# Optimization experiments

Measured on AMD Instinct MI355X. Metric: run time of the kernel, lower is better.

Reference implementation:

```python
import jax, jax.numpy as jnp
import numpy as np

DIM = 128
NUM_HEADS = 8
HEAD_DIM = DIM // NUM_HEADS
SCALE = HEAD_DIM ** -0.5


def setup_inputs() -> dict:
    key = jax.random.key(0)
    k0, k1, k2, k3 = jax.random.split(key, 4)
    B, N, C, H, W = 4, 8, DIM, 96, 96
    features = jax.random.normal(k0, (B, N, C, H, W), dtype=jnp.float32)
    w_qkv = jax.random.normal(k1, (C, 3 * C), dtype=jnp.float32) * (C ** -0.5)
    w_proj = jax.random.normal(k2, (C, C), dtype=jnp.float32) * (C ** -0.5)
    b_proj = jax.random.normal(k3, (C,), dtype=jnp.float32) * 0.02
    gamma = jnp.ones((C,), dtype=jnp.float32)
    beta = jnp.zeros((C,), dtype=jnp.float32)
    return {"features": features, "w_qkv": w_qkv, "w_proj": w_proj,
            "b_proj": b_proj, "gamma": gamma, "beta": beta}


def _layernorm(x, gamma, beta, eps=1e-5):
    mu = jnp.mean(x, axis=-1, keepdims=True)
    var = jnp.mean(jnp.square(x - mu), axis=-1, keepdims=True)
    return (x - mu) * jax.lax.rsqrt(var + eps) * gamma + beta


def reference(features, w_qkv, w_proj, b_proj, gamma, beta):
    B, N, C, H, W = features.shape
    residual = features
    # (B,N,C,H,W) -> (B*H*W, N, C)
    x = jnp.transpose(features, (0, 3, 4, 1, 2)).reshape(B * H * W, N, C)
    x = _layernorm(x, gamma, beta)
    qkv = (x @ w_qkv).reshape(B * H * W, N, 3, NUM_HEADS, HEAD_DIM)
    qkv = jnp.transpose(qkv, (2, 0, 3, 1, 4))  # (3, P, h, N, d)
    q, k, v = qkv[0], qkv[1], qkv[2]
    attn = jnp.einsum('phnd,phmd->phnm', q, k) * SCALE
    attn = jax.nn.softmax(attn, axis=-1)
    out = jnp.einsum('phnm,phmd->phnd', attn, v)  # (P, h, N, d)
    out = jnp.transpose(out, (0, 2, 1, 3)).reshape(B * H * W, N, C)
    out = out @ w_proj + b_proj
    out = out.reshape(B, H, W, N, C).transpose(0, 3, 4, 1, 2)
    return residual + out
```

## Files before the change

### kernel.cpp

```cpp
#include <hip/hip_runtime.h>

#define NFR 8
#define CDIM 128
#define HH 96
#define WW 96
#define NB 4
#define HWSZ 9216
#define NBLK 2304
#define NXCD 8
#define CPX (NBLK / NXCD)

typedef __attribute__((ext_vector_type(8))) short bf16x8;
typedef __attribute__((ext_vector_type(4))) float f32x4;
typedef __attribute__((ext_vector_type(2))) float f32x2;
typedef __attribute__((ext_vector_type(2))) __bf16 bf16x2;

union FragU { uint4 u; bf16x8 v; };

__device__ inline float bf2f(unsigned short h) {
    unsigned int x = ((unsigned int)h) << 16;
    float f; __builtin_memcpy(&f, &x, 4); return f;
}
__device__ inline unsigned short f2bf(float f) {
    unsigned int x; __builtin_memcpy(&x, &f, 4);
    return (unsigned short)((x + 0x7FFFu + ((x >> 16) & 1u)) >> 16);
}
__device__ inline unsigned int packbf(float a, float b) {
    return (unsigned int)f2bf(a) | ((unsigned int)f2bf(b) << 16);
}
__device__ inline unsigned int cvt2(float a, float b) {
    f32x2 f = {a, b};
    bf16x2 h = __builtin_convertvector(f, bf16x2);
    unsigned int u; __builtin_memcpy(&u, &h, 4); return u;
}
__device__ inline unsigned short cvt1(float a) {
    __bf16 h = (__bf16)a;
    unsigned short s; __builtin_memcpy(&s, &h, 2); return s;
}
__device__ inline int posmap(int c5) {
    return (c5 < 16) ? (((c5 >> 2) << 3) + (c5 & 3))
                     : ((((c5 & 15) >> 2) << 3) + 4 + (c5 & 3));
}

__global__ __launch_bounds__(256)
void repack_k(const float* __restrict__ wqkv, const float* __restrict__ wproj,
              const float* __restrict__ gamma, const float* __restrict__ beta,
              unsigned short* __restrict__ ws)
{
    int gid = blockIdx.x * 256 + threadIdx.x;
    uint4* wsq = (uint4*)ws;
    int l = gid & 63, lr = l & 15, lg = (l >> 4) & 3;
    if (gid < 8192) {
        int unit = gid >> 6;
        int col, ks, stride;
        float scale = 1.0f;
        const float* src;
        if (unit < 64) {
            int t = unit >> 2; ks = unit & 3;
            int hd = t >> 1, three = t & 1;
            col = three * 128 + hd * 16 + lr;
            src = wqkv; stride = 384;
            if (three == 0) scale = 0.25f;
        } else if (unit < 96) {
            int u2 = unit - 64; int hd = u2 >> 2; ks = u2 & 3;
            col = 256 + hd * 16 + lr;
            src = wqkv; stride = 384;
        } else {
            int u3 = unit - 96; int nt = u3 >> 2; ks = u3 & 3;
            col = nt * 16 + lr;
            src = wproj; stride = 128;
        }
        unsigned int dw[4];
        #pragma unroll
        for (int i = 0; i < 4; ++i) {
            int e0 = 2 * i, e1 = 2 * i + 1;
            int c0 = ks * 32 + lg * 4 + (e0 & 3) + ((e0 >> 2) << 4);
            int c1 = ks * 32 + lg * 4 + (e1 & 3) + ((e1 >> 2) << 4);
            dw[i] = packbf(src[c0 * stride + col] * scale, src[c1 * stride + col] * scale);
        }
        uint4 o; o.x = dw[0]; o.y = dw[1]; o.z = dw[2]; o.w = dw[3];
        wsq[gid] = o;
    } else if (gid < 8192 + 256) {
        int p = gid - 8192;
        int pp = p & 127;
        int ks = pp >> 5, pos = pp & 31;
        int c = ks * 32 + ((pos >> 3) << 2) + (pos & 3) + (((pos >> 2) & 1) << 4);
        ((float*)ws)[32768 + p] = (p < 128) ? gamma[c] : beta[c];
    }
}

__device__ inline f32x4 attn_ov(f32x4 q, f32x4 k, f32x4 v, bool valid) {
    FragU qb, kb, vb;
    qb.u.x = cvt2(q.x, q.y); qb.u.y = cvt2(q.z, q.w); qb.u.z = 0; qb.u.w = 0;
    kb.u.x = cvt2(k.x, k.y); kb.u.y = cvt2(k.z, k.w); kb.u.z = 0; kb.u.w = 0;
    vb.u.x = cvt2(v.x, v.y); vb.u.y = cvt2(v.z, v.w); vb.u.z = 0; vb.u.w = 0;
    f32x4 zz = {0,0,0,0};
    f32x4 st = __builtin_amdgcn_mfma_f32_16x16x32_bf16(kb.v, qb.v, zz, 0, 0, 0);
    float sc0 = st.x, sc1 = st.y, sc2 = st.z, sc3 = st.w;
    float m = valid ? fmaxf(fmaxf(sc0, sc1), fmaxf(sc2, sc3)) : -3.0e38f;
    m = fmaxf(m, __shfl_xor(m, 16));
    float e0 = valid ? __expf(sc0 - m) : 0.f, e1 = valid ? __expf(sc1 - m) : 0.f;
    float e2 = valid ? __expf(sc2 - m) : 0.f, e3 = valid ? __expf(sc3 - m) : 0.f;
    float sm = e0 + e1 + e2 + e3; sm += __shfl_xor(sm, 16);
    float inv = 1.f / sm;
    FragU pb;
    pb.u.x = cvt2(valid ? e0 * inv : 0.f, valid ? e1 * inv : 0.f);
    pb.u.y = cvt2(valid ? e2 * inv : 0.f, valid ? e3 * inv : 0.f);
    pb.u.z = 0; pb.u.w = 0;
    return __builtin_amdgcn_mfma_f32_16x16x32_bf16(vb.v, pb.v, zz, 0, 0, 0);
}

__global__ __launch_bounds__(256, 3)
void cfa_main(const float* __restrict__ feat, const float* __restrict__ bproj,
              const unsigned short* __restrict__ ws, float* __restrict__ outp)
{
    __shared__ uint4 xlnU4[2048];
    unsigned short* xln16 = (unsigned short*)xlnU4;
    unsigned int*   xln32 = (unsigned int*)xlnU4;

    const int tid = threadIdx.x;
    const int blk = (int)(blockIdx.x % NXCD) * CPX + (int)blockIdx.x / NXCD;
    const int wt = blk % 6, h = (blk / 6) % 96, b = blk / (6 * 96);
    const int base = ((b * NFR) * CDIM) * HWSZ + h * WW + wt * 16;

    #pragma unroll
    for (int it = 0; it < 8; ++it) {
        int t = it * 256 + tid;
        int pq = t & 3;
        int pr = t >> 2;
        int n = pr >> 6;
        int c = (pr & 63) * 2;
        const float* src = feat + base + (n * CDIM + c) * HWSZ + pq * 4;
        float4 f0 = *(const float4*)src;
        float4 f1 = *(const float4*)(src + HWSZ);
        int ks = c >> 5;
        int pos = posmap(c & 31);
        const float* a0 = (const float*)&f0;
        const float* a1 = (const float*)&f1;
        #pragma unroll
        for (int j = 0; j < 4; ++j) {
            int p = pq * 4 + j;
            int g = p >> 3, pin = p & 7;
            xln32[(g * 8192 + ks * 2048 + (pin * 8 + n) * 32 + pos) >> 1] =
                cvt2(a0[j], a1[j]);
        }
    }
    __syncthreads();

    const int wv = tid >> 6, l = tid & 63, lr = l & 15, lg = l >> 4;
    const uint4* wsq = (const uint4*)ws;

    uint4 Ac[4], Bc[4], Vc[4];
    #pragma unroll
    for (int ks = 0; ks < 4; ++ks) {
        Ac[ks] = wsq[(0 * 8 + ks) * 64 + l];
        Bc[ks] = wsq[(0 * 8 + 4 + ks) * 64 + l];
        Vc[ks] = wsq[4096 + ks * 64 + l];
    }

    {
        const float* gP = (const float*)ws + 32768;
        const float* bP = gP + 128;
        int rr = tid >> 2, ks = tid & 3;
        #pragma unroll
        for (int g = 0; g < 2; ++g) {
            int baseq = g * 1024 + ks * 256 + rr * 4;
            uint4 ch[4];
            #pragma unroll
            for (int j = 0; j < 4; ++j) ch[j] = xlnU4[baseq + ((j + rr + ks) & 3)];
            float s = 0.f, ss = 0.f;
            #pragma unroll
            for (int j = 0; j < 4; ++j) {
                const unsigned short* e = (const unsigned short*)&ch[j];
                #pragma unroll
                for (int b8 = 0; b8 < 8; ++b8) { float x = bf2f(e[b8]); s += x; ss += x * x; }
            }
            s += __shfl_xor(s, 1); ss += __shfl_xor(ss, 1);
            s += __shfl_xor(s, 2); ss += __shfl_xor(ss, 2);
            float mu = s * (1.f / 128.f);
            float var = ss * (1.f / 128.f) - mu * mu;
            float rstd = rsqrtf(var + 1e-5f);
            #pragma unroll
            for (int j = 0; j < 4; ++j) {
                int cj = (j + rr + ks) & 3;
                const unsigned short* e = (const unsigned short*)&ch[j];
                unsigned int dw[4];
                #pragma unroll
                for (int i = 0; i < 4; ++i) {
                    int p0 = cj * 8 + 2 * i, p1 = p0 + 1;
                    float x0 = (bf2f(e[2 * i])     - mu) * rstd * gP[ks * 32 + p0] + bP[ks * 32 + p0];
                    float x1 = (bf2f(e[2 * i + 1]) - mu) * rstd * gP[ks * 32 + p1] + bP[ks * 32 + p1];
                    dw[i] = cvt2(x0, x1);
                }
                uint4 o; o.x = dw[0]; o.y = dw[1]; o.z = dw[2]; o.w = dw[3];
                xlnU4[baseq + cj] = o;
            }
        }
    }

    FragU xf0[4], xf1[4];
    #pragma unroll
    for (int ks = 0; ks < 4; ++ks) {
        xf0[ks].u = xlnU4[ks * 256 + (wv * 16 + lr) * 4 + lg];
        xf1[ks].u = xlnU4[1024 + ks * 256 + (wv * 16 + lr) * 4 + lg];
    }
    __syncthreads();

    const bool valid = ((lg >> 1) == (lr >> 3));
    FragU pa0[4], pa1[4];
    #pragma unroll
    for (int ks = 0; ks < 4; ++ks) {
        pa0[ks].u.x = 0; pa0[ks].u.y = 0; pa0[ks].u.z = 0; pa0[ks].u.w = 0;
        pa1[ks].u.x = 0; pa1[ks].u.y = 0; pa1[ks].u.z = 0; pa1[ks].u.w = 0;
    }

    uint4 PBc[4];
    float biasc;
    #pragma unroll
    for (int hd = 0; hd < 8; ++hd) {
        uint4 An[4], Bn[4], Vn[4];
        if (hd < 7) {
            #pragma unroll
            for (int ks = 0; ks < 4; ++ks) {
                An[ks] = wsq[((hd + 1) * 8 + ks) * 64 + l];
                Bn[ks] = wsq[((hd + 1) * 8 + 4 + ks) * 64 + l];
                Vn[ks] = wsq[4096 + ((hd + 1) * 4 + ks) * 64 + l];
            }
        } else {
            #pragma unroll
            for (int ks = 0; ks < 4; ++ks) PBc[ks] = wsq[6144 + ks * 64 + l];
            biasc = bproj[lr];
        }
        f32x4 q0 = {0,0,0,0}, k0 = {0,0,0,0}, v0 = {0,0,0,0};
        f32x4 q1 = {0,0,0,0}, k1 = {0,0,0,0}, v1 = {0,0,0,0};
        #pragma unroll
        for (int ks = 0; ks < 4; ++ks) {
            FragU A, B, V2; A.u = Ac[ks]; B.u = Bc[ks]; V2.u = Vc[ks];
            q0 = __builtin_amdgcn_mfma_f32_16x16x32_bf16(A.v,  xf0[ks].v, q0, 0, 0, 0);
            k0 = __builtin_amdgcn_mfma_f32_16x16x32_bf16(B.v,  xf0[ks].v, k0, 0, 0, 0);
            q1 = __builtin_amdgcn_mfma_f32_16x16x32_bf16(A.v,  xf1[ks].v, q1, 0, 0, 0);
            k1 = __builtin_amdgcn_mfma_f32_16x16x32_bf16(B.v,  xf1[ks].v, k1, 0, 0, 0);
            v0 = __builtin_amdgcn_mfma_f32_16x16x32_bf16(xf0[ks].v, V2.v, v0, 0, 0, 0);
            v1 = __builtin_amdgcn_mfma_f32_16x16x32_bf16(xf1[ks].v, V2.v, v1, 0, 0, 0);
        }
        f32x4 o0 = attn_ov(q0, k0, v0, valid);
        f32x4 o1 = attn_ov(q1, k1, v1, valid);
        if ((hd & 1) == 0) {
            pa0[hd >> 1].u.x = cvt2(o0.x, o0.y); pa0[hd >> 1].u.y = cvt2(o0.z, o0.w);
            pa1[hd >> 1].u.x = cvt2(o1.x, o1.y); pa1[hd >> 1].u.y = cvt2(o1.z, o1.w);
        } else {
            pa0[hd >> 1].u.z = cvt2(o0.x, o0.y); pa0[hd >> 1].u.w = cvt2(o0.z, o0.w);
            pa1[hd >> 1].u.z = cvt2(o1.x, o1.y); pa1[hd >> 1].u.w = cvt2(o1.z, o1.w);
        }
        if (hd < 7) {
            #pragma unroll
            for (int ks = 0; ks < 4; ++ks) { Ac[ks] = An[ks]; Bc[ks] = Bn[ks]; Vc[ks] = Vn[ks]; }
        }
    }

    unsigned short* out_t = xln16;
    #pragma unroll
    for (int nt = 0; nt < 8; ++nt) {
        uint4 PBn[4]; float biasn;
        if (nt < 7) {
            #pragma unroll
            for (int ks = 0; ks < 4; ++ks) PBn[ks] = wsq[6144 + ((nt + 1) * 4 + ks) * 64 + l];
            biasn = bproj[(nt + 1) * 16 + lr];
        }
        f32x4 a0 = {0,0,0,0}, a1 = {0,0,0,0};
        #pragma unroll
        for (int ks = 0; ks < 4; ++ks) {
            FragU B; B.u = PBc[ks];
            a0 = __builtin_amdgcn_mfma_f32_16x16x32_bf16(pa0[ks].v, B.v, a0, 0, 0, 0);
            a1 = __builtin_amdgcn_mfma_f32_16x16x32_bf16(pa1[ks].v, B.v, a1, 0, 0, 0);
        }
        int col = nt * 16 + lr;
        #pragma unroll
        for (int j = 0; j < 4; ++j) {
            int row = wv * 16 + lg * 4 + j;
            int n = row & 7, p = row >> 3;
            out_t[n * 1024 + (col ^ n) * 8 + p]        = cvt1(a0[j] + biasc);
            out_t[8192 + n * 1024 + (col ^ n) * 8 + p] = cvt1(a1[j] + biasc);
        }
        if (nt < 7) {
            #pragma unroll
            for (int ks = 0; ks < 4; ++ks) PBc[ks] = PBn[ks];
            biasc = biasn;
        }
    }
    __syncthreads();
    #pragma unroll 4
    for (int it = 0; it < 16; ++it) {
        int t = it * 256 + tid;
        int pq = t & 3;
        int row = t >> 2;
        int n = row >> 7, c = row & 127;
        int gaddr = base + (n * CDIM + c) * HWSZ + pq * 4;
        float4 r0 = *(const float4*)(feat + gaddr);
        int p = pq * 4;
        int idx = (p >> 3) * 8192 + n * 1024 + (c ^ n) * 8 + (p & 7);
        uint2 tv = *(const uint2*)(out_t + idx);
        const unsigned short* tp = (const unsigned short*)&tv;
        float4 o;
        o.x = r0.x + bf2f(tp[0]); o.y = r0.y + bf2f(tp[1]);
        o.z = r0.z + bf2f(tp[2]); o.w = r0.w + bf2f(tp[3]);
        *(float4*)(outp + gaddr) = o;
    }
}

extern "C" void kernel_launch(void* const* d_in, const int* in_sizes, int n_in,
                              void* d_out, int out_size, void* d_ws, size_t ws_size,
                              hipStream_t stream) {
    const float* feat  = (const float*)d_in[0];
    const float* wqkv  = (const float*)d_in[1];
    const float* wproj = (const float*)d_in[2];
    const float* bproj = (const float*)d_in[3];
    const float* gamma = (const float*)d_in[4];
    const float* beta  = (const float*)d_in[5];
    unsigned short* ws = (unsigned short*)d_ws;
    float* outp = (float*)d_out;

    hipLaunchKernelGGL(repack_k, dim3(33), dim3(256), 0, stream,
                       wqkv, wproj, gamma, beta, ws);
    hipLaunchKernelGGL(cfa_main, dim3(NBLK), dim3(256), 0, stream,
                       feat, bproj, ws, outp);
}
```

Baseline: 114.6 us.

## Fuse LayerNorm into MFMA register fragments and prefetch residual before projection

LayerNorm now runs on each wave's MFMA input fragments in registers, using cross-lane shuffles for the statistics. This removes the shared-memory read/normalize/write pass and one barrier. Gamma and beta are pre-packed as bf16 fragments in the repack kernel, which adds a little rounding. The residual feature reads are issued into 16 float4 registers before the output projection so their latency overlaps the projection MFMAs. That raises register pressure under launch_bounds(256,3).

```diff
diff --git a/kernel.cpp b/kernel.cpp
--- a/kernel.cpp
+++ b/kernel.cpp
@@ -80,12 +80,22 @@
         }
         uint4 o; o.x = dw[0]; o.y = dw[1]; o.z = dw[2]; o.w = dw[3];
         wsq[gid] = o;
-    } else if (gid < 8192 + 256) {
-        int p = gid - 8192;
-        int pp = p & 127;
-        int ks = pp >> 5, pos = pp & 31;
-        int c = ks * 32 + ((pos >> 3) << 2) + (pos & 3) + (((pos >> 2) & 1) << 4);
-        ((float*)ws)[32768 + p] = (p < 128) ? gamma[c] : beta[c];
+    } else if (gid < 8192 + 32) {
+        int t = gid - 8192;
+        int isb = t >> 4;
+        int unit = t & 15;
+        int ks2 = unit >> 2, lg2 = unit & 3;
+        const float* src2 = isb ? beta : gamma;
+        unsigned int dw[4];
+        #pragma unroll
+        for (int i = 0; i < 4; ++i) {
+            int e0 = 2 * i, e1 = 2 * i + 1;
+            int c0 = ks2 * 32 + lg2 * 4 + (e0 & 3) + ((e0 >> 2) << 4);
+            int c1 = ks2 * 32 + lg2 * 4 + (e1 & 3) + ((e1 >> 2) << 4);
+            dw[i] = packbf(src2[c0], src2[c1]);
+        }
+        uint4 o; o.x = dw[0]; o.y = dw[1]; o.z = dw[2]; o.w = dw[3];
+        wsq[8192 + t] = o;
     }
 }
 
@@ -110,6 +120,37 @@
     return __builtin_amdgcn_mfma_f32_16x16x32_bf16(vb.v, pb.v, zz, 0, 0, 0);
 }
 
+__device__ inline void ln_reg(FragU* xf, const uint4* gf, const uint4* bfr) {
+    float s = 0.f, ss = 0.f;
+    #pragma unroll
+    for (int ks = 0; ks < 4; ++ks) {
+        const unsigned short* e = (const unsigned short*)&xf[ks];
+        #pragma unroll
+        for (int j = 0; j < 8; ++j) { float x = bf2f(e[j]); s += x; ss += x * x; }
+    }
+    s += __shfl_xor(s, 16); ss += __shfl_xor(ss, 16);
+    s += __shfl_xor(s, 32); ss += __shfl_xor(ss, 32);
+    float mu = s * (1.f / 128.f);
+    float var = ss * (1.f / 128.f) - mu * mu;
+    float rstd = rsqrtf(var + 1e-5f);
+    float mr = mu * rstd;
+    #pragma unroll
+    for (int ks = 0; ks < 4; ++ks) {
+        const unsigned short* e = (const unsigned short*)&xf[ks];
+        const unsigned short* g = (const unsigned short*)&gf[ks];
+        const unsigned short* b = (const unsigned short*)&bfr[ks];
+        unsigned int dw[4];
+        #pragma unroll
+        for (int i = 0; i < 4; ++i) {
+            float x0 = bf2f(e[2 * i])     * rstd - mr;
+            float x1 = bf2f(e[2 * i + 1]) * rstd - mr;
+            dw[i] = cvt2(x0 * bf2f(g[2 * i])     + bf2f(b[2 * i]),
+                         x1 * bf2f(g[2 * i + 1]) + bf2f(b[2 * i + 1]));
+        }
+        xf[ks].u.x = dw[0]; xf[ks].u.y = dw[1]; xf[ks].u.z = dw[2]; xf[ks].u.w = dw[3];
+    }
+}
+
 __global__ __launch_bounds__(256, 3)
 void cfa_main(const float* __restrict__ feat, const float* __restrict__ bproj,
               const unsigned short* __restrict__ ws, float* __restrict__ outp)
@@ -150,52 +191,14 @@
     const int wv = tid >> 6, l = tid & 63, lr = l & 15, lg = l >> 4;
     const uint4* wsq = (const uint4*)ws;
 
-    uint4 Ac[4], Bc[4], Vc[4];
+    uint4 Ac[4], Bc[4], Vc[4], gf[4], bfx[4];
     #pragma unroll
     for (int ks = 0; ks < 4; ++ks) {
         Ac[ks] = wsq[(0 * 8 + ks) * 64 + l];
         Bc[ks] = wsq[(0 * 8 + 4 + ks) * 64 + l];
         Vc[ks] = wsq[4096 + ks * 64 + l];
-    }
-
-    {
-        const float* gP = (const float*)ws + 32768;
-        const float* bP = gP + 128;
-        int rr = tid >> 2, ks = tid & 3;
-        #pragma unroll
-        for (int g = 0; g < 2; ++g) {
-            int baseq = g * 1024 + ks * 256 + rr * 4;
-            uint4 ch[4];
-            #pragma unroll
-            for (int j = 0; j < 4; ++j) ch[j] = xlnU4[baseq + ((j + rr + ks) & 3)];
-            float s = 0.f, ss = 0.f;
-            #pragma unroll
-            for (int j = 0; j < 4; ++j) {
-                const unsigned short* e = (const unsigned short*)&ch[j];
-                #pragma unroll
-                for (int b8 = 0; b8 < 8; ++b8) { float x = bf2f(e[b8]); s += x; ss += x * x; }
-            }
-            s += __shfl_xor(s, 1); ss += __shfl_xor(ss, 1);
-            s += __shfl_xor(s, 2); ss += __shfl_xor(ss, 2);
-            float mu = s * (1.f / 128.f);
-            float var = ss * (1.f / 128.f) - mu * mu;
-            float rstd = rsqrtf(var + 1e-5f);
-            #pragma unroll
-            for (int j = 0; j < 4; ++j) {
-                int cj = (j + rr + ks) & 3;
-                const unsigned short* e = (const unsigned short*)&ch[j];
-                unsigned int dw[4];
-                #pragma unroll
-                for (int i = 0; i < 4; ++i) {
-                    int p0 = cj * 8 + 2 * i, p1 = p0 + 1;
-                    float x0 = (bf2f(e[2 * i])     - mu) * rstd * gP[ks * 32 + p0] + bP[ks * 32 + p0];
-                    float x1 = (bf2f(e[2 * i + 1]) - mu) * rstd * gP[ks * 32 + p1] + bP[ks * 32 + p1];
-                    dw[i] = cvt2(x0, x1);
-                }
-                uint4 o; o.x = dw[0]; o.y = dw[1]; o.z = dw[2]; o.w = dw[3];
-                xlnU4[baseq + cj] = o;
-            }
-        }
+        gf[ks]  = wsq[8192 + ks * 4 + lg];
+        bfx[ks] = wsq[8208 + ks * 4 + lg];
     }
 
     FragU xf0[4], xf1[4];
@@ -204,7 +207,8 @@
         xf0[ks].u = xlnU4[ks * 256 + (wv * 16 + lr) * 4 + lg];
         xf1[ks].u = xlnU4[1024 + ks * 256 + (wv * 16 + lr) * 4 + lg];
     }
-    __syncthreads();
+    ln_reg(xf0, gf, bfx);
+    ln_reg(xf1, gf, bfx);
 
     const bool valid = ((lg >> 1) == (lr >> 3));
     FragU pa0[4], pa1[4];
@@ -258,6 +262,18 @@
         }
     }
 
+    float4 R[16];
+    #pragma unroll
+    for (int it = 0; it < 16; ++it) {
+        int t = it * 256 + tid;
+        int pq = t & 3;
+        int row = t >> 2;
+        int n = row >> 7, c = row & 127;
+        R[it] = *(const float4*)(feat + base + (n * CDIM + c) * HWSZ + pq * 4);
+    }
+
+    __syncthreads();
+
     unsigned short* out_t = xln16;
     #pragma unroll
     for (int nt = 0; nt < 8; ++nt) {
@@ -289,21 +305,21 @@
         }
     }
     __syncthreads();
-    #pragma unroll 4
+
+    #pragma unroll
     for (int it = 0; it < 16; ++it) {
         int t = it * 256 + tid;
         int pq = t & 3;
         int row = t >> 2;
         int n = row >> 7, c = row & 127;
         int gaddr = base + (n * CDIM + c) * HWSZ + pq * 4;
-        float4 r0 = *(const float4*)(feat + gaddr);
         int p = pq * 4;
         int idx = (p >> 3) * 8192 + n * 1024 + (c ^ n) * 8 + (p & 7);
         uint2 tv = *(const uint2*)(out_t + idx);
         const unsigned short* tp = (const unsigned short*)&tv;
         float4 o;
-        o.x = r0.x + bf2f(tp[0]); o.y = r0.y + bf2f(tp[1]);
-        o.z = r0.z + bf2f(tp[2]); o.w = r0.w + bf2f(tp[3]);
+        o.x = R[it].x + bf2f(tp[0]); o.y = R[it].y + bf2f(tp[1]);
+        o.z = R[it].z + bf2f(tp[2]); o.w = R[it].w + bf2f(tp[3]);
         *(float4*)(outp + gaddr) = o;
     }
 }
```

After: 196.0 us. 71.0% more time.
